# Kernel optimization log

Hardware: AMD Instinct MI355X
Metric: run time of the kernel (lower is better)

## Reference

```python
import jax, jax.numpy as jnp
import numpy as np

B, C, H, W = 16, 3, 1024, 1024
DENSITY = 0.015
SIGMA = 1.5
K = 5  # blur kernel size
N_FLAKES = int(H * W * DENSITY)  # 15728


def setup_inputs() -> dict:
    key = jax.random.key(0)
    kx, ky, kxs, kr = jax.random.split(key, 4)
    x = jax.random.uniform(kx, (B, C, H, W), dtype=jnp.float32)
    ys = jax.random.randint(ky, (B, N_FLAKES), 0, H, dtype=jnp.int32)
    xs = jax.random.randint(kxs, (B, N_FLAKES), 0, W, dtype=jnp.int32)
    rs = jax.random.randint(kr, (B, N_FLAKES), 1, 4, dtype=jnp.int32)  # radius in {1,2,3}
    return {"x": x, "ys": ys, "xs": xs, "rs": rs}


def reference(x, ys, xs, rs):
    Bb, Cc, Hh, Ww = x.shape
    # --- vectorized flake stamping (replaces per-flake Python loop) ---
    # Each flake writes a (2r+1)x(2r+1) square of 0.95, clipped to image bounds.
    # Max radius is 3 -> enumerate the 7x7 = 49 candidate offsets per flake.
    off = jnp.arange(-3, 4)
    dyg, dxg = jnp.meshgrid(off, off, indexing="ij")
    dy = dyg.reshape(-1)  # [49]
    dx = dxg.reshape(-1)  # [49]
    r = rs[..., None]  # [B, N, 1]
    valid = (jnp.abs(dy) <= r) & (jnp.abs(dx) <= r)  # [B, N, 49]
    # Clamping out-of-bounds coords to the border is equivalent to torch's
    # slice-clipping because the written value is a constant (0.95) and the
    # border pixel is already covered by an in-range offset. Invalid offsets
    # (|d| > r) are redirected to the flake center, which is always stamped.
    yy = jnp.where(valid, jnp.clip(ys[..., None] + dy, 0, Hh - 1), ys[..., None])
    xx = jnp.where(valid, jnp.clip(xs[..., None] + dx, 0, Ww - 1), xs[..., None])
    b = jnp.arange(Bb)[:, None, None]  # [B,1,1]
    out = x.at[b, :, yy, xx].set(0.95)  # stamp all channels

    # --- depthwise 5x5 gaussian blur ---
    coords = jnp.arange(K, dtype=jnp.float32) - K // 2
    g = jnp.exp(-(coords ** 2) / (2.0 * SIGMA ** 2))
    g = g / g.sum()
    kern = jnp.outer(g, g).astype(x.dtype)[None, None]  # [1,1,5,5]
    kern = jnp.broadcast_to(kern, (Cc, 1, K, K))  # depthwise: O=C, I=1
    pad = K // 2
    out = jax.lax.conv_general_dilated(
        out, kern, window_strides=(1, 1), padding=[(pad, pad), (pad, pad)],
        feature_group_count=Cc, dimension_numbers=("NCHW", "OIHW", "NCHW"))
    return jnp.clip(out, 0.0, 1.0)
```

## Files before the change

### kernel.cpp

```cpp
#include <hip/hip_runtime.h>


#define H_ 1024
#define W_ 1024
#define B_ 16
#define C_ 3
#define NF_ 15728
#define MASK_WORDS_PER_B (H_ * W_ / 32)

#define G0 0.12007838f
#define G1 0.23388076f
#define G2 0.29208172f

typedef float nat_f4 __attribute__((ext_vector_type(4)));

__global__ void clear_mask_kernel(uint4* __restrict__ mask, int n4) {
    int i = blockIdx.x * blockDim.x + threadIdx.x;
    if (i < n4) mask[i] = make_uint4(0u, 0u, 0u, 0u);
}

__global__ void stamp_kernel(const int* __restrict__ ys, const int* __restrict__ xs,
                             const int* __restrict__ rs, unsigned int* __restrict__ mask) {
    int t = blockIdx.x * blockDim.x + threadIdx.x;
    if (t >= B_ * NF_) return;
    int b = t / NF_;
    int y0 = ys[t], x0 = xs[t], r = rs[t];
    unsigned int* mb = mask + b * MASK_WORDS_PER_B;
    int xlo = max(x0 - r, 0), xhi = min(x0 + r, W_ - 1);
    int ylo = max(y0 - r, 0), yhi = min(y0 + r, H_ - 1);
    for (int y = ylo; y <= yhi; ++y) {
        int i0 = (y << 10) + xlo;
        int i1 = (y << 10) + xhi;
        int w0 = i0 >> 5, w1 = i1 >> 5;
        unsigned int m0 = ~0u << (i0 & 31);
        unsigned int m1 = ~0u >> (31 - (i1 & 31));
        if (w0 == w1) {
            atomicOr(mb + w0, m0 & m1);
        } else {
            atomicOr(mb + w0, m0);
            atomicOr(mb + w1, m1);
        }
    }
}

constexpr int BAND = 8;
constexpr int ROWS = BAND + 4;

__global__ __launch_bounds__(256, 4) void blur_kernel(const float* __restrict__ x,
                                                      const unsigned int* __restrict__ mask,
                                                      float* __restrict__ out) {
    const int plane = blockIdx.z;
    const int b = plane / C_;
    const float* xp = x + (size_t)plane * (H_ * W_);
    float* op = out + (size_t)plane * (H_ * W_);
    const unsigned int* mb = mask + b * MASK_WORDS_PER_B;

    const int tid = threadIdx.x;
    const int wv = tid >> 6;
    const int ln = tid & 63;
    const int gx4 = (wv << 8) + (ln << 2);
    const int y0 = blockIdx.y * BAND;

    const bool isL = (ln == 0), isR = (ln == 63);
    const int hoff = isL ? gx4 - 2 : gx4 + 4;
    const bool haloOn = (isL || isR) && ((unsigned)hoff < (unsigned)W_);
    const int mwi = gx4 >> 5, mbit = gx4 & 31;
    const int hwi = hoff >> 5, hbit = hoff & 31;

    float4 raw[ROWS];
    float2 hraw[ROWS];
    unsigned int rm[ROWS], hrm[ROWS];

    #pragma unroll
    for (int r = 0; r < ROWS; ++r) {
        int gy = y0 - 2 + r;
        if ((unsigned)gy < (unsigned)H_) {
            raw[r] = *(const float4*)(xp + (gy << 10) + gx4);
            rm[r]  = mb[(gy << 5) + mwi];
            if (haloOn) {
                hraw[r] = *(const float2*)(xp + (gy << 10) + hoff);
                hrm[r]  = mb[(gy << 5) + hwi];
            } else { hraw[r] = make_float2(0.f, 0.f); hrm[r] = 0u; }
        } else {
            raw[r] = make_float4(0.f, 0.f, 0.f, 0.f); rm[r] = 0u;
            hraw[r] = make_float2(0.f, 0.f); hrm[r] = 0u;
        }
    }

    #pragma unroll
    for (int r = 0; r < ROWS; ++r) {
        unsigned int m = rm[r];
        if ((m >> (mbit + 0)) & 1u) raw[r].x = 0.95f;
        if ((m >> (mbit + 1)) & 1u) raw[r].y = 0.95f;
        if ((m >> (mbit + 2)) & 1u) raw[r].z = 0.95f;
        if ((m >> (mbit + 3)) & 1u) raw[r].w = 0.95f;
        unsigned int hm = hrm[r];
        if ((hm >> (hbit + 0)) & 1u) hraw[r].x = 0.95f;
        if ((hm >> (hbit + 1)) & 1u) hraw[r].y = 0.95f;
    }

    #pragma unroll
    for (int t = 0; t < BAND; ++t) {
        float4 vb;
        vb.x = G0 * (raw[t].x + raw[t + 4].x) + G1 * (raw[t + 1].x + raw[t + 3].x) + G2 * raw[t + 2].x;
        vb.y = G0 * (raw[t].y + raw[t + 4].y) + G1 * (raw[t + 1].y + raw[t + 3].y) + G2 * raw[t + 2].y;
        vb.z = G0 * (raw[t].z + raw[t + 4].z) + G1 * (raw[t + 1].z + raw[t + 3].z) + G2 * raw[t + 2].z;
        vb.w = G0 * (raw[t].w + raw[t + 4].w) + G1 * (raw[t + 1].w + raw[t + 3].w) + G2 * raw[t + 2].w;
        float2 hvb;
        hvb.x = G0 * (hraw[t].x + hraw[t + 4].x) + G1 * (hraw[t + 1].x + hraw[t + 3].x) + G2 * hraw[t + 2].x;
        hvb.y = G0 * (hraw[t].y + hraw[t + 4].y) + G1 * (hraw[t + 1].y + hraw[t + 3].y) + G2 * hraw[t + 2].y;

        float az = __shfl_up(vb.z, 1u);
        float aw = __shfl_up(vb.w, 1u);
        float cx = __shfl_down(vb.x, 1u);
        float cy = __shfl_down(vb.y, 1u);
        az = isL ? hvb.x : az;  aw = isL ? hvb.y : aw;
        cx = isR ? hvb.x : cx;  cy = isR ? hvb.y : cy;

        float4 o;
        o.x = G0 * (az + vb.z) + G1 * (aw + vb.y) + G2 * vb.x;
        o.y = G0 * (aw + vb.w) + G1 * (vb.x + vb.z) + G2 * vb.y;
        o.z = G0 * (vb.x + cx) + G1 * (vb.y + vb.w) + G2 * vb.z;
        o.w = G0 * (vb.y + cy) + G1 * (vb.z + cx) + G2 * vb.w;
        o.x = fminf(fmaxf(o.x, 0.0f), 1.0f);
        o.y = fminf(fmaxf(o.y, 0.0f), 1.0f);
        o.z = fminf(fmaxf(o.z, 0.0f), 1.0f);
        o.w = fminf(fmaxf(o.w, 0.0f), 1.0f);

        nat_f4 ov;
        ov.x = o.x; ov.y = o.y; ov.z = o.z; ov.w = o.w;
        __builtin_nontemporal_store(ov, (nat_f4*)(op + ((y0 + t) << 10) + gx4));
    }
}

extern "C" void kernel_launch(void* const* d_in, const int* in_sizes, int n_in,
                              void* d_out, int out_size, void* d_ws, size_t ws_size,
                              hipStream_t stream) {
    const float* x  = (const float*)d_in[0];
    const int*   ys = (const int*)d_in[1];
    const int*   xs = (const int*)d_in[2];
    const int*   rs = (const int*)d_in[3];
    float* out = (float*)d_out;
    unsigned int* mask = (unsigned int*)d_ws;

    int n4 = B_ * MASK_WORDS_PER_B / 4;
    clear_mask_kernel<<<dim3((n4 + 255) / 256), dim3(256), 0, stream>>>((uint4*)mask, n4);

    int nst = B_ * NF_;
    stamp_kernel<<<dim3((nst + 255) / 256), dim3(256), 0, stream>>>(ys, xs, rs, mask);

    dim3 grid(1, H_ / BAND, B_ * C_);
    blur_kernel<<<grid, dim3(256), 0, stream>>>(x, mask, out);
}
```

Before: 406.6 us.

## Share wave-edge halos via LDS and swizzle blur block order

Edge lanes of each wavefront no longer reload 2-pixel halo columns and mask words from global memory. Each wave writes its vertically blurred boundary columns to shared memory, and neighbouring waves read them after a barrier. The grid is also flattened to 1D with a swizzle that spreads consecutive blocks across planes, likely aiming at XCD/channel locality. This saves divergent halo loads and halo arithmetic at the cost of an LDS round-trip, a __syncthreads, and an extra pass over the rows.

```diff
diff --git a/kernel.cpp b/kernel.cpp
--- a/kernel.cpp
+++ b/kernel.cpp
@@ -45,11 +45,17 @@
 
 constexpr int BAND = 8;
 constexpr int ROWS = BAND + 4;
+constexpr int NYB = H_ / BAND;
+constexpr int NWG = NYB * B_ * C_;
 
 __global__ __launch_bounds__(256, 4) void blur_kernel(const float* __restrict__ x,
                                                       const unsigned int* __restrict__ mask,
                                                       float* __restrict__ out) {
-    const int plane = blockIdx.z;
+    const int bid = blockIdx.x;
+    const int swz = (bid & 7) * (NWG / 8) + (bid >> 3);
+    const int plane = swz >> 7;
+    const int yband = swz & 127;
+
     const int b = plane / C_;
     const float* xp = x + (size_t)plane * (H_ * W_);
     float* op = out + (size_t)plane * (H_ * W_);
@@ -59,17 +65,15 @@
     const int wv = tid >> 6;
     const int ln = tid & 63;
     const int gx4 = (wv << 8) + (ln << 2);
-    const int y0 = blockIdx.y * BAND;
+    const int y0 = yband * BAND;
 
     const bool isL = (ln == 0), isR = (ln == 63);
-    const int hoff = isL ? gx4 - 2 : gx4 + 4;
-    const bool haloOn = (isL || isR) && ((unsigned)hoff < (unsigned)W_);
     const int mwi = gx4 >> 5, mbit = gx4 & 31;
-    const int hwi = hoff >> 5, hbit = hoff & 31;
 
     float4 raw[ROWS];
-    float2 hraw[ROWS];
-    unsigned int rm[ROWS], hrm[ROWS];
+    unsigned int rm[ROWS];
+
+    __shared__ float2 edges[4][BAND][2];
 
     #pragma unroll
     for (int r = 0; r < ROWS; ++r) {
@@ -77,13 +81,8 @@
         if ((unsigned)gy < (unsigned)H_) {
             raw[r] = *(const float4*)(xp + (gy << 10) + gx4);
             rm[r]  = mb[(gy << 5) + mwi];
-            if (haloOn) {
-                hraw[r] = *(const float2*)(xp + (gy << 10) + hoff);
-                hrm[r]  = mb[(gy << 5) + hwi];
-            } else { hraw[r] = make_float2(0.f, 0.f); hrm[r] = 0u; }
         } else {
             raw[r] = make_float4(0.f, 0.f, 0.f, 0.f); rm[r] = 0u;
-            hraw[r] = make_float2(0.f, 0.f); hrm[r] = 0u;
         }
     }
 
@@ -94,9 +93,6 @@
         if ((m >> (mbit + 1)) & 1u) raw[r].y = 0.95f;
         if ((m >> (mbit + 2)) & 1u) raw[r].z = 0.95f;
         if ((m >> (mbit + 3)) & 1u) raw[r].w = 0.95f;
-        unsigned int hm = hrm[r];
-        if ((hm >> (hbit + 0)) & 1u) hraw[r].x = 0.95f;
-        if ((hm >> (hbit + 1)) & 1u) hraw[r].y = 0.95f;
     }
 
     #pragma unroll
@@ -106,17 +102,27 @@
         vb.y = G0 * (raw[t].y + raw[t + 4].y) + G1 * (raw[t + 1].y + raw[t + 3].y) + G2 * raw[t + 2].y;
         vb.z = G0 * (raw[t].z + raw[t + 4].z) + G1 * (raw[t + 1].z + raw[t + 3].z) + G2 * raw[t + 2].z;
         vb.w = G0 * (raw[t].w + raw[t + 4].w) + G1 * (raw[t + 1].w + raw[t + 3].w) + G2 * raw[t + 2].w;
-        float2 hvb;
-        hvb.x = G0 * (hraw[t].x + hraw[t + 4].x) + G1 * (hraw[t + 1].x + hraw[t + 3].x) + G2 * hraw[t + 2].x;
-        hvb.y = G0 * (hraw[t].y + hraw[t + 4].y) + G1 * (hraw[t + 1].y + hraw[t + 3].y) + G2 * hraw[t + 2].y;
+        if (isL) edges[wv][t][0] = make_float2(vb.x, vb.y);
+        if (isR) edges[wv][t][1] = make_float2(vb.z, vb.w);
+        raw[t] = vb;
+    }
+    __syncthreads();
 
+    #pragma unroll
+    for (int t = 0; t < BAND; ++t) {
+        float4 vb = raw[t];
         float az = __shfl_up(vb.z, 1u);
         float aw = __shfl_up(vb.w, 1u);
         float cx = __shfl_down(vb.x, 1u);
         float cy = __shfl_down(vb.y, 1u);
-        az = isL ? hvb.x : az;  aw = isL ? hvb.y : aw;
-        cx = isR ? hvb.x : cx;  cy = isR ? hvb.y : cy;
-
+        if (isL) {
+            if (wv > 0) { float2 e = edges[wv - 1][t][1]; az = e.x; aw = e.y; }
+            else        { az = 0.f; aw = 0.f; }
+        }
+        if (isR) {
+            if (wv < 3) { float2 e = edges[wv + 1][t][0]; cx = e.x; cy = e.y; }
+            else        { cx = 0.f; cy = 0.f; }
+        }
         float4 o;
         o.x = G0 * (az + vb.z) + G1 * (aw + vb.y) + G2 * vb.x;
         o.y = G0 * (aw + vb.w) + G1 * (vb.x + vb.z) + G2 * vb.y;
@@ -149,6 +155,5 @@
     int nst = B_ * NF_;
     stamp_kernel<<<dim3((nst + 255) / 256), dim3(256), 0, stream>>>(ys, xs, rs, mask);
 
-    dim3 grid(1, H_ / BAND, B_ * C_);
-    blur_kernel<<<grid, dim3(256), 0, stream>>>(x, mask, out);
+    blur_kernel<<<dim3(NWG), dim3(256), 0, stream>>>(x, mask, out);
 }
```

Result: no change. 401.4 us (-1.3%).
